# Kernel optimization log

Hardware: AMD Instinct MI355X
Metric: run time of the kernel (lower is better)

Reference implementation:

```python
import jax, jax.numpy as jnp
import numpy as np

B, N_ATOM, N_TOK = 1, 1536, 384
C_ATOM, C_PAIR, C_TOK = 128, 16, 384
C_HID, H, L = 32, 4, 3
HID = 2 * C_ATOM  # n_transition = 2
N_QUERY, N_KEY, INF = 32, 128, 1e9


def _ln(x, gamma=None, beta=None, eps=1e-5):
    mu = jnp.mean(x, axis=-1, keepdims=True)
    var = jnp.mean(jnp.square(x - mu), axis=-1, keepdims=True)
    y = (x - mu) * jax.lax.rsqrt(var + eps)
    if gamma is not None:
        y = y * gamma
    if beta is not None:
        y = y + beta
    return y


def _adaln(a, s, gamma_s, Wg, bg, Ws):
    an = _ln(a)            # LN without affine
    sn = _ln(s, gamma_s)   # scale-only LN
    return jax.nn.sigmoid(sn @ Wg + bg) * an + sn @ Ws


def _block_mask():
    # AtomTransformer.forward: 32-query x 128-key block-local mask
    offset = N_QUERY // 2 - 0.5
    n_center = N_ATOM // N_QUERY + 1
    centers = offset + jnp.arange(n_center, dtype=jnp.float32) * N_QUERY
    idx = jnp.arange(N_ATOM, dtype=jnp.float32)[:, None]
    row = (jnp.abs(idx - centers[None, :]) < N_QUERY / 2).astype(jnp.float32)
    col = (jnp.abs(idx - centers[None, :]) < N_KEY / 2).astype(jnp.float32)
    return (row @ col.T - 1.0) * INF   # [N,N]: 0 in-window, -INF outside


def _forward(ref_pos, ref_mask, ref_element, ref_charge, ref_atom_name_chars,
             ref_space_uid, token_mask, atom_to_token_index,
             W_feats, W_ref_offset, W_inv_sq, W_valid, W_l, W_m,
             W_mlp1, W_mlp2, W_mlp3, W_out_tok,
             attn_ada_gamma_s, attn_ada_Wg, attn_ada_bg, attn_ada_Ws,
             Wq, bq, Wk, Wv, lnz_g, lnz_b, Wb, Wgate, Wo, Wsg, bsg,
             tr_ada_gamma_s, tr_ada_Wg, tr_ada_bg, tr_ada_Ws,
             tr_W1, tr_W2, tr_Wog, tr_bog, tr_Wout):
    # --- RefAtomFeatureEmbedder (AF3 Alg 5 lines 1-6) ---
    feats = jnp.concatenate([
        ref_pos, ref_mask[..., None], ref_element, ref_charge[..., None],
        ref_atom_name_chars.reshape(B, N_ATOM, -1), ref_space_uid[..., None]], axis=-1)
    cl = feats @ W_feats                                     # [B,N,C_ATOM]
    d = ref_pos[:, None, :, :] - ref_pos[:, :, None, :]      # d[l,m] = pos[m]-pos[l]
    v = (ref_space_uid[:, None, :] == ref_space_uid[:, :, None]).astype(jnp.float32)[..., None]
    plm = (d @ W_ref_offset) * v
    inv_sq = 1.0 / (1.0 + jnp.sum(d * d, axis=-1, keepdims=True))
    plm = plm + (inv_sq @ W_inv_sq) * v + (v @ W_valid) * v  # [B,N,N,C_PAIR]
    ql = cl
    # --- single -> pair conditioning + pair MLP ---
    crelu = jax.nn.relu(cl)
    plm = plm + (crelu @ W_l)[:, :, None, :] + (crelu @ W_m)[:, None, :, :]
    h = jax.nn.relu(plm) @ W_mlp1
    h = jax.nn.relu(h) @ W_mlp2
    h = jax.nn.relu(h) @ W_mlp3
    plm = plm + h
    # --- AtomTransformer (Alg 7) -> DiffusionTransformer (Alg 23) ---
    beta = _block_mask()                                     # [N,N]
    atom_mask = jnp.einsum('blt,bt->bl', atom_to_token_index, token_mask)
    mask_bias = (atom_mask - 1.0)[:, None, None, :] * INF    # [B,1,1,N]
    a, s = ql, cl
    inv_sqrt = 1.0 / np.sqrt(C_HID)
    for i in range(L):
        # AttentionPairBias (Alg 24)
        an = _adaln(a, s, attn_ada_gamma_s[i], attn_ada_Wg[i], attn_ada_bg[i], attn_ada_Ws[i])
        q = (an @ Wq[i] + bq[i]).reshape(B, N_ATOM, H, C_HID)
        k = (an @ Wk[i]).reshape(B, N_ATOM, H, C_HID)
        vv = (an @ Wv[i]).reshape(B, N_ATOM, H, C_HID)
        zb = _ln(plm, lnz_g[i], lnz_b[i]) @ Wb[i]            # [B,N,N,H]
        logits = (jnp.einsum('bqhc,bkhc->bhqk', q, k) * inv_sqrt
                  + jnp.moveaxis(zb, -1, 1) + beta[None, None] + mask_bias)
        A = jax.nn.softmax(logits, axis=-1)
        o = jnp.einsum('bhqk,bkhc->bqhc', A, vv)
        g = jax.nn.sigmoid(an @ Wgate[i]).reshape(B, N_ATOM, H, C_HID)
        o = (g * o).reshape(B, N_ATOM, H * C_HID) @ Wo[i]
        attn_out = jax.nn.sigmoid(s @ Wsg[i] + bsg[i]) * o
        # ConditionedTransitionBlock (Alg 25) on pre-attention a (Alg 23)
        tn = _adaln(a, s, tr_ada_gamma_s[i], tr_ada_Wg[i], tr_ada_bg[i], tr_ada_Ws[i])
        hh = jax.nn.silu(tn @ tr_W1[i]) * (tn @ tr_W2[i])
        tr_out = jax.nn.sigmoid(s @ tr_Wog[i] + tr_bog[i]) * (hh @ tr_Wout[i])
        a = attn_out + tr_out
    # --- mean-aggregate atoms -> tokens (Alg 5 line 15) ---
    al = jax.nn.relu(a @ W_out_tok)                          # [B,N,C_TOK]
    counts = jnp.maximum(jnp.sum(atom_to_token_index, axis=1), 1.0)
    a_tok = jnp.einsum('blt,blc->btc', atom_to_token_index, al) / counts[..., None]
    return a_tok


def setup_inputs() -> dict:
    key = jax.random.key(0)
    ks = iter(jax.random.split(key, 80))

    def nrm(shape, scale=0.02):
        return jax.random.normal(next(ks), shape, dtype=jnp.float32) * scale

    inp = {}
    inp['ref_pos'] = jax.random.normal(next(ks), (B, N_ATOM, 3), dtype=jnp.float32) * 3.0
    inp['ref_mask'] = jnp.ones((B, N_ATOM), jnp.float32)
    elem = jax.random.randint(next(ks), (B, N_ATOM), 0, 128)
    inp['ref_element'] = jax.nn.one_hot(elem, 128, dtype=jnp.float32)
    inp['ref_charge'] = jax.random.normal(next(ks), (B, N_ATOM), dtype=jnp.float32)
    chars = jax.random.randint(next(ks), (B, N_ATOM, 4), 0, 64)
    inp['ref_atom_name_chars'] = jax.nn.one_hot(chars, 64, dtype=jnp.float32)
    inp['ref_space_uid'] = jnp.broadcast_to(
        (jnp.arange(N_ATOM) // 8).astype(jnp.float32), (B, N_ATOM))
    inp['token_mask'] = jnp.ones((B, N_TOK), jnp.float32)
    tok = (jnp.arange(N_ATOM) * N_TOK) // N_ATOM  # ~4 atoms per token
    inp['atom_to_token_index'] = jnp.broadcast_to(
        jax.nn.one_hot(tok, N_TOK, dtype=jnp.float32), (B, N_ATOM, N_TOK))
    # embedder params
    inp['W_feats'] = nrm((390, C_ATOM))
    inp['W_ref_offset'] = nrm((3, C_PAIR))
    inp['W_inv_sq'] = nrm((1, C_PAIR))
    inp['W_valid'] = nrm((1, C_PAIR))
    inp['W_l'] = nrm((C_ATOM, C_PAIR))
    inp['W_m'] = nrm((C_ATOM, C_PAIR))
    inp['W_mlp1'] = nrm((C_PAIR, C_PAIR))
    inp['W_mlp2'] = nrm((C_PAIR, C_PAIR))
    inp['W_mlp3'] = nrm((C_PAIR, C_PAIR))
    inp['W_out_tok'] = nrm((C_ATOM, C_TOK))
    # DiffusionTransformer params, stacked over L blocks
    inp['attn_ada_gamma_s'] = jnp.ones((L, C_ATOM), jnp.float32)
    inp['attn_ada_Wg'] = nrm((L, C_ATOM, C_ATOM))
    inp['attn_ada_bg'] = jnp.zeros((L, C_ATOM), jnp.float32)
    inp['attn_ada_Ws'] = nrm((L, C_ATOM, C_ATOM))
    inp['Wq'] = nrm((L, C_ATOM, H * C_HID))
    inp['bq'] = jnp.zeros((L, H * C_HID), jnp.float32)
    inp['Wk'] = nrm((L, C_ATOM, H * C_HID))
    inp['Wv'] = nrm((L, C_ATOM, H * C_HID))
    inp['lnz_g'] = jnp.ones((L, C_PAIR), jnp.float32)
    inp['lnz_b'] = jnp.zeros((L, C_PAIR), jnp.float32)
    inp['Wb'] = nrm((L, C_PAIR, H))
    inp['Wgate'] = nrm((L, C_ATOM, H * C_HID))
    inp['Wo'] = nrm((L, H * C_HID, C_ATOM))
    inp['Wsg'] = nrm((L, C_ATOM, C_ATOM))
    inp['bsg'] = jnp.full((L, C_ATOM), -2.0, jnp.float32)
    inp['tr_ada_gamma_s'] = jnp.ones((L, C_ATOM), jnp.float32)
    inp['tr_ada_Wg'] = nrm((L, C_ATOM, C_ATOM))
    inp['tr_ada_bg'] = jnp.zeros((L, C_ATOM), jnp.float32)
    inp['tr_ada_Ws'] = nrm((L, C_ATOM, C_ATOM))
    inp['tr_W1'] = nrm((L, C_ATOM, HID))
    inp['tr_W2'] = nrm((L, C_ATOM, HID))
    inp['tr_Wog'] = nrm((L, C_ATOM, C_ATOM))
    inp['tr_bog'] = jnp.full((L, C_ATOM), -2.0, jnp.float32)
    inp['tr_Wout'] = nrm((L, HID, C_ATOM))
    return inp


def reference(ref_pos, ref_mask, ref_element, ref_charge, ref_atom_name_chars,
              ref_space_uid, token_mask, atom_to_token_index,
              W_feats, W_ref_offset, W_inv_sq, W_valid, W_l, W_m,
              W_mlp1, W_mlp2, W_mlp3, W_out_tok,
              attn_ada_gamma_s, attn_ada_Wg, attn_ada_bg, attn_ada_Ws,
              Wq, bq, Wk, Wv, lnz_g, lnz_b, Wb, Wgate, Wo, Wsg, bsg,
              tr_ada_gamma_s, tr_ada_Wg, tr_ada_bg, tr_ada_Ws,
              tr_W1, tr_W2, tr_Wog, tr_bog, tr_Wout):
    return _forward(ref_pos, ref_mask, ref_element, ref_charge, ref_atom_name_chars,
                    ref_space_uid, token_mask, atom_to_token_index,
                    W_feats, W_ref_offset, W_inv_sq, W_valid, W_l, W_m,
                    W_mlp1, W_mlp2, W_mlp3, W_out_tok,
                    attn_ada_gamma_s, attn_ada_Wg, attn_ada_bg, attn_ada_Ws,
                    Wq, bq, Wk, Wv, lnz_g, lnz_b, Wb, Wgate, Wo, Wsg, bsg,
                    tr_ada_gamma_s, tr_ada_Wg, tr_ada_bg, tr_ada_Ws,
                    tr_W1, tr_W2, tr_Wog, tr_bog, tr_Wout)
```

## Files before the change

kernel.cpp:

```cpp
#include <hip/hip_runtime.h>
#include <math.h>

#define N_ATOM 1536
#define NB     48
#define NLAYER 3
#define NC     196608L
#define ZSTRIDE 786432L

struct GD { const float* A; const float* B; float* C; const float* ks; const float* bias;
            int act; int ldb; int ldc; int _pad; };
struct GB { GD g[18]; };

__global__ __launch_bounds__(128) void embed_tok_kernel(
    const float* __restrict__ pos, const float* __restrict__ rmask,
    const float* __restrict__ elem, const float* __restrict__ charge,
    const float* __restrict__ chars, const float* __restrict__ uid,
    const float* __restrict__ Wf, const float* __restrict__ W_l, const float* __restrict__ W_m,
    const float* __restrict__ a2t, const float* __restrict__ tmask,
    float* __restrict__ cl, float* __restrict__ aa, float* __restrict__ clnorm,
    float* __restrict__ pl, float* __restrict__ pm,
    int* __restrict__ tok, float* __restrict__ amask)
{
  int l = blockIdx.x, c = threadIdx.x;
  __shared__ int sidx[6];
  __shared__ float red[128];
  __shared__ float crow[128];
  if (elem[(long)l * 128 + c] > 0.5f) sidx[0] = c;
  float v0 = chars[(long)l * 256 + c];
  if (v0 > 0.5f) sidx[1 + (c >> 6)] = c & 63;
  float v1 = chars[(long)l * 256 + 128 + c];
  if (v1 > 0.5f) sidx[3 + (c >> 6)] = c & 63;
  for (int j = c; j < 384; j += 128)
    if (a2t[(long)l * 384 + j] > 0.5f) sidx[5] = j;
  __syncthreads();
  float acc = pos[l * 3 + 0] * Wf[c]
            + pos[l * 3 + 1] * Wf[128 + c]
            + pos[l * 3 + 2] * Wf[256 + c]
            + rmask[l] * Wf[384 + c]
            + Wf[(4 + sidx[0]) * 128 + c]
            + charge[l] * Wf[132 * 128 + c]
            + Wf[(133 + sidx[1]) * 128 + c]
            + Wf[(197 + sidx[2]) * 128 + c]
            + Wf[(261 + sidx[3]) * 128 + c]
            + Wf[(325 + sidx[4]) * 128 + c]
            + uid[l] * Wf[389 * 128 + c];
  long gi = (long)l * 128 + c;
  cl[gi] = acc; aa[gi] = acc; crow[c] = fmaxf(acc, 0.f);
  red[c] = acc; __syncthreads();
  for (int s = 64; s > 0; s >>= 1) { if (c < s) red[c] += red[c + s]; __syncthreads(); }
  float mu = red[0] * (1.f / 128.f); __syncthreads();
  float d = acc - mu; red[c] = d * d; __syncthreads();
  for (int s = 64; s > 0; s >>= 1) { if (c < s) red[c] += red[c + s]; __syncthreads(); }
  clnorm[gi] = d * rsqrtf(red[0] * (1.f / 128.f) + 1e-5f);
  if (c < 32) {
    const float* W = (c < 16) ? W_l : W_m;
    int o = c & 15;
    float s = 0.f;
    for (int cc = 0; cc < 128; cc++) s = fmaf(crow[cc], W[cc * 16 + o], s);
    if (c < 16) pl[l * 16 + o] = s; else pm[l * 16 + o] = s;
  }
  if (c == 127) {
    int j = sidx[5];
    tok[l] = j; amask[l] = tmask[j];
  }
}

__global__ __launch_bounds__(128) void adaln_kernel(
    const float* __restrict__ a,
    const float* __restrict__ sgA, const float* __restrict__ adA,
    const float* __restrict__ sgT, const float* __restrict__ adT,
    float* __restrict__ an, float* __restrict__ tn)
{
  __shared__ float red[128];
  int l = blockIdx.x, c = threadIdx.x;
  float x = a[(long)l * 128 + c];
  red[c] = x; __syncthreads();
  for (int s = 64; s > 0; s >>= 1) { if (c < s) red[c] += red[c + s]; __syncthreads(); }
  float mu = red[0] * (1.f / 128.f); __syncthreads();
  float d = x - mu; red[c] = d * d; __syncthreads();
  for (int s = 64; s > 0; s >>= 1) { if (c < s) red[c] += red[c + s]; __syncthreads(); }
  float nv = d * rsqrtf(red[0] * (1.f / 128.f) + 1e-5f);
  long i = (long)l * 128 + c;
  an[i] = sgA[i] * nv + adA[i];
  tn[i] = sgT[i] * nv + adT[i];
}

__device__ __forceinline__ void gemm64_body(float* sm, const float* A, const float* B, float* C,
                                            const float* ks, const float* bias, int act,
                                            int ldb, int ldc, int row0, int col0) {
  float* As = sm; float* Bs = sm + 2176;
  int tid = threadIdx.x;
  int tx = tid & 15, ty = tid >> 4;
  float acc[4][4] = {};
  for (int k0 = 0; k0 < 128; k0 += 32) {
    __syncthreads();
    { int r = tid >> 3, k4 = tid & 7;
#pragma unroll
      for (int half = 0; half < 2; half++) {
        int row = r + half * 32;
        float4 v = *(const float4*)(A + (long)(row0 + row) * 128 + k0 + k4 * 4);
        if (ks) { const float* kp = ks + k0 + k4 * 4; v.x *= kp[0]; v.y *= kp[1]; v.z *= kp[2]; v.w *= kp[3]; }
        As[(k4 * 4 + 0) * 68 + row] = v.x; As[(k4 * 4 + 1) * 68 + row] = v.y;
        As[(k4 * 4 + 2) * 68 + row] = v.z; As[(k4 * 4 + 3) * 68 + row] = v.w;
      } }
    { int kk = tid >> 4, n4 = tid & 15;
#pragma unroll
      for (int half = 0; half < 2; half++) {
        int k = kk + half * 16;
        *(float4*)&Bs[k * 68 + n4 * 4] = *(const float4*)(B + (long)(k0 + k) * ldb + col0 + n4 * 4);
      } }
    __syncthreads();
#pragma unroll
    for (int kk = 0; kk < 32; kk++) {
      float4 a = *(const float4*)&As[kk * 68 + ty * 4];
      float4 b = *(const float4*)&Bs[kk * 68 + tx * 4];
      float av[4] = {a.x, a.y, a.z, a.w}, bv[4] = {b.x, b.y, b.z, b.w};
#pragma unroll
      for (int i = 0; i < 4; i++)
#pragma unroll
        for (int j = 0; j < 4; j++) acc[i][j] = fmaf(av[i], bv[j], acc[i][j]);
    }
  }
  __syncthreads();
#pragma unroll
  for (int i = 0; i < 4; i++) {
    int row = row0 + ty * 4 + i;
#pragma unroll
    for (int j = 0; j < 4; j++) {
      int col = col0 + tx * 4 + j;
      float x = acc[i][j];
      if (bias) x += bias[col];
      if (act == 1) x = 1.f / (1.f + expf(-x));
      else if (act == 2) x = fmaxf(x, 0.f);
      C[(long)row * ldc + col] = x;
    }
  }
}

__global__ __launch_bounds__(256) void gemm64(GB args, int M)
{
  __shared__ float sm[4352];
  GD d = args.g[blockIdx.z];
  gemm64_body(sm, d.A, d.B, d.C, d.ks, d.bias, d.act, d.ldb, d.ldc, blockIdx.y * 64, blockIdx.x * 64);
}

__global__ __launch_bounds__(256) void zpre_kernel(
    const float* __restrict__ pos, const float* __restrict__ uid,
    const float* __restrict__ Wro, const float* __restrict__ Winv, const float* __restrict__ Wval,
    const float* __restrict__ M1, const float* __restrict__ M2, const float* __restrict__ M3,
    const float* __restrict__ Lg, const float* __restrict__ Lb, const float* __restrict__ Wb,
    const float* __restrict__ pl, const float* __restrict__ pm, float* __restrict__ zb,
    GB ba)
{
  __shared__ float sm[4352];
  int bid = blockIdx.x, tid = threadIdx.x;
  if (bid >= 768) {
    int u = bid - 768;
    GD d = ba.g[u / 48];
    int tt = u % 48;
    gemm64_body(sm, d.A, d.B, d.C, d.ks, d.bias, d.act, d.ldb, d.ldc, (tt >> 1) * 64, (tt & 1) * 64);
    return;
  }
  if (tid < 48)  sm[tid] = Wro[tid];
  if (tid < 16)  { sm[48 + tid] = Winv[tid]; sm[64 + tid] = Wval[tid]; }
  sm[80 + tid] = M1[tid]; sm[336 + tid] = M2[tid]; sm[592 + tid] = M3[tid];
  if (tid < 48)  { sm[848 + tid] = Lg[tid]; sm[896 + tid] = Lb[tid]; }
  if (tid < 192) sm[944 + tid] = Wb[tid];
  __syncthreads();
  const float* sWro = sm;      const float* sWinv = sm + 48;  const float* sWval = sm + 64;
  const float* sM1 = sm + 80;  const float* sM2 = sm + 336;   const float* sM3 = sm + 592;
  const float* sLg = sm + 848; const float* sLb = sm + 896;   const float* sWb = sm + 944;
  int b = bid >> 4;
  int pc = (bid & 15) * 256 + tid;
  int qi = pc >> 7, kj = pc & 127;
  int l = b * 32 + qi, m = b * 32 - 48 + kj;
  long base = (long)(b * 32 + qi) * 128 + kj;
  if (m < 0 || m >= N_ATOM) {
    for (int i = 0; i < NLAYER; i++)
      for (int h = 0; h < 4; h++) zb[i * ZSTRIDE + h * NC + base] = 0.f;
    return;
  }
  float dx = pos[m * 3 + 0] - pos[l * 3 + 0];
  float dy = pos[m * 3 + 1] - pos[l * 3 + 1];
  float dz = pos[m * 3 + 2] - pos[l * 3 + 2];
  float v = (uid[m] == uid[l]) ? 1.f : 0.f;
  float inv = 1.f / (1.f + dx * dx + dy * dy + dz * dz);
  float pv[16], ha[16], hb[16];
#pragma unroll
  for (int j = 0; j < 16; j++)
    pv[j] = v * (dx * sWro[j] + dy * sWro[16 + j] + dz * sWro[32 + j] + inv * sWinv[j] + sWval[j])
            + pl[l * 16 + j] + pm[m * 16 + j];
#pragma unroll
  for (int jo = 0; jo < 16; jo++) { float s = 0.f; for (int ji = 0; ji < 16; ji++) s = fmaf(fmaxf(pv[ji], 0.f), sM1[ji * 16 + jo], s); ha[jo] = s; }
#pragma unroll
  for (int jo = 0; jo < 16; jo++) { float s = 0.f; for (int ji = 0; ji < 16; ji++) s = fmaf(fmaxf(ha[ji], 0.f), sM2[ji * 16 + jo], s); hb[jo] = s; }
#pragma unroll
  for (int jo = 0; jo < 16; jo++) { float s = 0.f; for (int ji = 0; ji < 16; ji++) s = fmaf(fmaxf(hb[ji], 0.f), sM3[ji * 16 + jo], s); ha[jo] = s; }
#pragma unroll
  for (int j = 0; j < 16; j++) pv[j] += ha[j];
  for (int i = 0; i < NLAYER; i++) {
    float mu = 0.f;
#pragma unroll
    for (int j = 0; j < 16; j++) mu += pv[j];
    mu *= (1.f / 16.f);
    float var = 0.f;
#pragma unroll
    for (int j = 0; j < 16; j++) { float dd = pv[j] - mu; var += dd * dd; }
    var *= (1.f / 16.f);
    float rs = rsqrtf(var + 1e-5f);
    float zn[16];
#pragma unroll
    for (int j = 0; j < 16; j++) zn[j] = (pv[j] - mu) * rs * sLg[i * 16 + j] + sLb[i * 16 + j];
    for (int h = 0; h < 4; h++) {
      float s = 0.f;
#pragma unroll
      for (int j = 0; j < 16; j++) s = fmaf(zn[j], sWb[i * 64 + j * 4 + h], s);
      zb[i * ZSTRIDE + h * NC + base] = s;
    }
  }
}

__global__ __launch_bounds__(256) void attn_kernel(
    const float* __restrict__ qb, const float* __restrict__ kb, const float* __restrict__ vb,
    const float* __restrict__ gb, const float* __restrict__ zb, const float* __restrict__ amask,
    float* __restrict__ go)
{
  __shared__ float qs[16][36], ks[128][36], vs[128][36], ps[16][132];
  int bx = blockIdx.x, h = blockIdx.y, t = threadIdx.x;
  int b = bx >> 1, half = bx & 1;
  int q0 = b * 32 + half * 16;
  int kbase = b * 32 - 48;
  const float* zbh = zb + (long)h * NC;
  if (t < 128) {
    int qi = t >> 3, c4 = t & 7;
    *(float4*)&qs[qi][c4 * 4] = *(const float4*)(qb + (long)(q0 + qi) * 128 + h * 32 + c4 * 4);
  }
  for (int idx = t; idx < 128 * 8; idx += 256) {
    int kj = idx >> 3, c4 = idx & 7;
    int m = kbase + kj;
    float4 kv = make_float4(0.f, 0.f, 0.f, 0.f), vv = make_float4(0.f, 0.f, 0.f, 0.f);
    if (m >= 0 && m < N_ATOM) {
      kv = *(const float4*)(kb + (long)m * 128 + h * 32 + c4 * 4);
      vv = *(const float4*)(vb + (long)m * 128 + h * 32 + c4 * 4);
    }
    *(float4*)&ks[kj][c4 * 4] = kv;
    *(float4*)&vs[kj][c4 * 4] = vv;
  }
  __syncthreads();
  const float isq = 0.17677669529663687f;
  for (int p = t; p < 2048; p += 256) {
    int qi = p >> 7, kj = p & 127;
    int m = kbase + kj;
    float s = 0.f;
#pragma unroll
    for (int c4 = 0; c4 < 8; c4++) {
      float4 a = *(const float4*)&qs[qi][c4 * 4];
      float4 k4 = *(const float4*)&ks[kj][c4 * 4];
      s = fmaf(a.x, k4.x, s); s = fmaf(a.y, k4.y, s);
      s = fmaf(a.z, k4.z, s); s = fmaf(a.w, k4.w, s);
    }
    float logit;
    if (m >= 0 && m < N_ATOM) {
      logit = s * isq + zbh[(long)(q0 + qi) * 128 + kj] + (amask[m] - 1.f) * 1e9f;
    } else {
      logit = -1e9f;
    }
    ps[qi][kj] = logit;
  }
  __syncthreads();
  {
    int row = t >> 4, ln = t & 15;
    float mx = -1e30f;
    for (int kj = ln; kj < 128; kj += 16) mx = fmaxf(mx, ps[row][kj]);
#pragma unroll
    for (int o = 8; o > 0; o >>= 1) mx = fmaxf(mx, __shfl_xor(mx, o));
    float sm = 0.f;
    for (int kj = ln; kj < 128; kj += 16) { float e = expf(ps[row][kj] - mx); ps[row][kj] = e; sm += e; }
#pragma unroll
    for (int o = 8; o > 0; o >>= 1) sm += __shfl_xor(sm, o);
    float r = 1.f / sm;
    for (int kj = ln; kj < 128; kj += 16) ps[row][kj] *= r;
  }
  __syncthreads();
  {
    int qi = t >> 4, seg = (t >> 3) & 1, c4 = t & 7;
    float4 acc = make_float4(0.f, 0.f, 0.f, 0.f);
    int kj0 = seg * 64;
#pragma unroll 4
    for (int kj = kj0; kj < kj0 + 64; kj++) {
      float p = ps[qi][kj];
      float4 v = *(const float4*)&vs[kj][c4 * 4];
      acc.x = fmaf(p, v.x, acc.x); acc.y = fmaf(p, v.y, acc.y);
      acc.z = fmaf(p, v.z, acc.z); acc.w = fmaf(p, v.w, acc.w);
    }
    acc.x += __shfl_xor(acc.x, 8);
    acc.y += __shfl_xor(acc.y, 8);
    acc.z += __shfl_xor(acc.z, 8);
    acc.w += __shfl_xor(acc.w, 8);
    if (seg == 0) {
      long gi = (long)(q0 + qi) * 128 + h * 32 + c4 * 4;
      float4 g = *(const float4*)(gb + gi);
      acc.x *= g.x; acc.y *= g.y; acc.z *= g.z; acc.w *= g.w;
      *(float4*)(go + gi) = acc;
    }
  }
}

__global__ __launch_bounds__(256) void gemm_dual32(
    const float* __restrict__ A1, const float* __restrict__ B1,
    const float* __restrict__ h1, const float* __restrict__ h2, const float* __restrict__ B2,
    const float* __restrict__ g1, const float* __restrict__ g2,
    float* __restrict__ C)
{
  __shared__ float As[32 * 36];
  __shared__ float Bs[32 * 68];
  const int N = 128;
  int t = threadIdx.x;
  int row0 = blockIdx.y * 32, col0 = blockIdx.x * 64;
  int tx = t & 15, ty = t >> 4;
  float acc1[2][4] = {}, acc2[2][4] = {};
  for (int k0 = 0; k0 < 128; k0 += 32) {
    __syncthreads();
    { int r = t >> 3, k4 = t & 7;
      float4 v = *(const float4*)(A1 + (long)(row0 + r) * 128 + k0 + k4 * 4);
      As[(k4 * 4 + 0) * 36 + r] = v.x; As[(k4 * 4 + 1) * 36 + r] = v.y;
      As[(k4 * 4 + 2) * 36 + r] = v.z; As[(k4 * 4 + 3) * 36 + r] = v.w;
    }
    for (int e = t; e < 512; e += 256) {
      int k = e >> 4, n4 = e & 15;
      *(float4*)&Bs[k * 68 + n4 * 4] = *(const float4*)(B1 + (long)(k0 + k) * N + col0 + n4 * 4);
    }
    __syncthreads();
#pragma unroll
    for (int kk = 0; kk < 32; kk++) {
      float a0 = As[kk * 36 + ty * 2], a1 = As[kk * 36 + ty * 2 + 1];
      float4 b = *(const float4*)&Bs[kk * 68 + tx * 4];
      float bv[4] = {b.x, b.y, b.z, b.w};
#pragma unroll
      for (int j = 0; j < 4; j++) {
        acc1[0][j] = fmaf(a0, bv[j], acc1[0][j]);
        acc1[1][j] = fmaf(a1, bv[j], acc1[1][j]);
      }
    }
  }
  for (int k0 = 0; k0 < 256; k0 += 32) {
    __syncthreads();
    { int r = t >> 3, k4 = t & 7;
      long o = (long)(row0 + r) * 256 + k0 + k4 * 4;
      float4 x = *(const float4*)(h1 + o);
      float4 y = *(const float4*)(h2 + o);
      As[(k4 * 4 + 0) * 36 + r] = (x.x / (1.f + expf(-x.x))) * y.x;
      As[(k4 * 4 + 1) * 36 + r] = (x.y / (1.f + expf(-x.y))) * y.y;
      As[(k4 * 4 + 2) * 36 + r] = (x.z / (1.f + expf(-x.z))) * y.z;
      As[(k4 * 4 + 3) * 36 + r] = (x.w / (1.f + expf(-x.w))) * y.w;
    }
    for (int e = t; e < 512; e += 256) {
      int k = e >> 4, n4 = e & 15;
      *(float4*)&Bs[k * 68 + n4 * 4] = *(const float4*)(B2 + (long)(k0 + k) * N + col0 + n4 * 4);
    }
    __syncthreads();
#pragma unroll
    for (int kk = 0; kk < 32; kk++) {
      float a0 = As[kk * 36 + ty * 2], a1 = As[kk * 36 + ty * 2 + 1];
      float4 b = *(const float4*)&Bs[kk * 68 + tx * 4];
      float bv[4] = {b.x, b.y, b.z, b.w};
#pragma unroll
      for (int j = 0; j < 4; j++) {
        acc2[0][j] = fmaf(a0, bv[j], acc2[0][j]);
        acc2[1][j] = fmaf(a1, bv[j], acc2[1][j]);
      }
    }
  }
#pragma unroll
  for (int i = 0; i < 2; i++) {
    long o = (long)(row0 + ty * 2 + i) * N + col0 + tx * 4;
    float4 ga = *(const float4*)(g1 + o);
    float4 gb = *(const float4*)(g2 + o);
    float4 r;
    r.x = ga.x * acc1[i][0] + gb.x * acc2[i][0];
    r.y = ga.y * acc1[i][1] + gb.y * acc2[i][1];
    r.z = ga.z * acc1[i][2] + gb.z * acc2[i][2];
    r.w = ga.w * acc1[i][3] + gb.w * acc2[i][3];
    *(float4*)(C + o) = r;
  }
}

__global__ __launch_bounds__(256) void gemm_scatter(
    const float* __restrict__ A, const float* __restrict__ B,
    const int* __restrict__ tok,
    float* __restrict__ out, int K)
{
  __shared__ float As[32][68];
  __shared__ float Bs[32][68];
  int tid = threadIdx.x;
  int row0 = blockIdx.y * 64, col0 = blockIdx.x * 64;
  int tx = tid & 15, ty = tid >> 4;
  float acc[4][4] = {};
  for (int k0 = 0; k0 < K; k0 += 32) {
    __syncthreads();
    { int r = tid >> 3, k4 = tid & 7;
#pragma unroll
      for (int half = 0; half < 2; half++) {
        int row = r + half * 32;
        float4 v = *(const float4*)(A + (long)(row0 + row) * K + k0 + k4 * 4);
        As[k4 * 4 + 0][row] = v.x; As[k4 * 4 + 1][row] = v.y;
        As[k4 * 4 + 2][row] = v.z; As[k4 * 4 + 3][row] = v.w;
      } }
    { int kk = tid >> 4, n4 = tid & 15;
#pragma unroll
      for (int half = 0; half < 2; half++) {
        int k = kk + half * 16;
        float4 v = *(const float4*)(B + (long)(k0 + k) * 384 + col0 + n4 * 4);
        *(float4*)&Bs[k][n4 * 4] = v;
      } }
    __syncthreads();
#pragma unroll
    for (int kk = 0; kk < 32; kk++) {
      float4 a = *(const float4*)&As[kk][ty * 4];
      float4 b = *(const float4*)&Bs[kk][tx * 4];
      float av[4] = {a.x, a.y, a.z, a.w}, bv[4] = {b.x, b.y, b.z, b.w};
#pragma unroll
      for (int i = 0; i < 4; i++)
#pragma unroll
        for (int j = 0; j < 4; j++) acc[i][j] = fmaf(av[i], bv[j], acc[i][j]);
    }
  }
  __syncthreads();
  int r0 = row0 + ty * 4;
  int t0 = tok[r0];
  int cnt = 0;
#pragma unroll
  for (int i = 0; i < 4; i++) cnt += (tok[r0 + i] == t0) ? 1 : 0;
  float inv = 1.f / fmaxf((float)cnt, 1.f);
#pragma unroll
  for (int j = 0; j < 4; j++) {
    int col = col0 + tx * 4 + j;
    float s = 0.f;
#pragma unroll
    for (int i = 0; i < 4; i++)
      if (tok[r0 + i] == t0) s += fmaxf(acc[i][j], 0.f);
    out[(long)t0 * 384 + col] = s * inv;
  }
}

extern "C" void kernel_launch(void* const* d_in, const int* in_sizes, int n_in,
                              void* d_out, int out_size, void* d_ws, size_t ws_size,
                              hipStream_t stream)
{
  const float* pos    = (const float*)d_in[0];
  const float* rmask  = (const float*)d_in[1];
  const float* elem   = (const float*)d_in[2];
  const float* charge = (const float*)d_in[3];
  const float* chars  = (const float*)d_in[4];
  const float* uid    = (const float*)d_in[5];
  const float* tmask  = (const float*)d_in[6];
  const float* a2t    = (const float*)d_in[7];
  const float* Wf     = (const float*)d_in[8];
  const float* Wro    = (const float*)d_in[9];
  const float* Winv   = (const float*)d_in[10];
  const float* Wval   = (const float*)d_in[11];
  const float* W_l    = (const float*)d_in[12];
  const float* W_m    = (const float*)d_in[13];
  const float* M1     = (const float*)d_in[14];
  const float* M2     = (const float*)d_in[15];
  const float* M3     = (const float*)d_in[16];
  const float* Wtok   = (const float*)d_in[17];
  const float* gA     = (const float*)d_in[18];
  const float* WgA    = (const float*)d_in[19];
  const float* bgA    = (const float*)d_in[20];
  const float* WsA    = (const float*)d_in[21];
  const float* Wq     = (const float*)d_in[22];
  const float* bq     = (const float*)d_in[23];
  const float* Wk     = (const float*)d_in[24];
  const float* Wv     = (const float*)d_in[25];
  const float* Lg     = (const float*)d_in[26];
  const float* Lb     = (const float*)d_in[27];
  const float* Wb     = (const float*)d_in[28];
  const float* Wgate  = (const float*)d_in[29];
  const float* Wo     = (const float*)d_in[30];
  const float* Wsg    = (const float*)d_in[31];
  const float* bsg    = (const float*)d_in[32];
  const float* gT     = (const float*)d_in[33];
  const float* WgT    = (const float*)d_in[34];
  const float* bgT    = (const float*)d_in[35];
  const float* WsT    = (const float*)d_in[36];
  const float* trW1   = (const float*)d_in[37];
  const float* trW2   = (const float*)d_in[38];
  const float* Wog    = (const float*)d_in[39];
  const float* bog    = (const float*)d_in[40];
  const float* Wout   = (const float*)d_in[41];
  float* out = (float*)d_out;

  float* ws = (float*)d_ws;
  size_t off = 0;
  auto alloc = [&](size_t n) { float* p = ws + off; off += n; return p; };
  float* cl     = alloc(NC);
  float* aa     = alloc(NC);
  float* clnorm = alloc(NC);
  float* an     = alloc(NC);
  float* tn     = alloc(NC);
  float* qbuf   = alloc(NC);
  float* kbuf   = alloc(NC);
  float* vbuf   = alloc(NC);
  float* gbuf   = alloc(NC);
  float* gobuf  = alloc(NC);
  float* h1     = alloc((size_t)N_ATOM * 256);
  float* h2     = alloc((size_t)N_ATOM * 256);
  float* pl     = alloc((size_t)N_ATOM * 16);
  float* pm     = alloc((size_t)N_ATOM * 16);
  float* zbias  = alloc((size_t)NLAYER * ZSTRIDE);
  float* sgA    = alloc(NC * NLAYER);
  float* adA    = alloc(NC * NLAYER);
  float* sgT    = alloc(NC * NLAYER);
  float* adT    = alloc(NC * NLAYER);
  float* gsg    = alloc(NC * NLAYER);
  float* gog    = alloc(NC * NLAYER);
  float* amask  = alloc(N_ATOM);
  int*   tok    = (int*)alloc(N_ATOM);
  (void)ws_size; (void)in_sizes; (void)n_in; (void)out_size;

  embed_tok_kernel<<<N_ATOM, 128, 0, stream>>>(pos, rmask, elem, charge, chars, uid, Wf,
                                               W_l, W_m, a2t, tmask,
                                               cl, aa, clnorm, pl, pm, tok, amask);

  {
    GB ba = {};
    for (int i = 0; i < NLAYER; i++) {
      size_t o = (size_t)i * NC;
      ba.g[i * 6 + 0] = { clnorm, WgA + i * 16384, sgA + o, gA + i * 128, bgA + i * 128, 1, 128, 128, 0 };
      ba.g[i * 6 + 1] = { clnorm, WsA + i * 16384, adA + o, gA + i * 128, nullptr,       0, 128, 128, 0 };
      ba.g[i * 6 + 2] = { clnorm, WgT + i * 16384, sgT + o, gT + i * 128, bgT + i * 128, 1, 128, 128, 0 };
      ba.g[i * 6 + 3] = { clnorm, WsT + i * 16384, adT + o, gT + i * 128, nullptr,       0, 128, 128, 0 };
      ba.g[i * 6 + 4] = { cl,     Wsg + i * 16384, gsg + o, nullptr,      bsg + i * 128, 1, 128, 128, 0 };
      ba.g[i * 6 + 5] = { cl,     Wog + i * 16384, gog + o, nullptr,      bog + i * 128, 1, 128, 128, 0 };
    }
    zpre_kernel<<<768 + 864, 256, 0, stream>>>(pos, uid, Wro, Winv, Wval, M1, M2, M3,
                                               Lg, Lb, Wb, pl, pm, zbias, ba);
  }

  for (int i = 0; i < NLAYER; i++) {
    size_t o = (size_t)i * NC;
    adaln_kernel<<<N_ATOM, 128, 0, stream>>>(aa, sgA + o, adA + o, sgT + o, adT + o, an, tn);
    {
      GB ba = {};
      ba.g[0] = { an, Wq + i * 16384,        qbuf, nullptr, bq + i * 128, 0, 128, 128, 0 };
      ba.g[1] = { an, Wk + i * 16384,        kbuf, nullptr, nullptr,      0, 128, 128, 0 };
      ba.g[2] = { an, Wv + i * 16384,        vbuf, nullptr, nullptr,      0, 128, 128, 0 };
      ba.g[3] = { an, Wgate + i * 16384,     gbuf, nullptr, nullptr,      1, 128, 128, 0 };
      ba.g[4] = { tn, trW1 + i * 32768,       h1,  nullptr, nullptr,      0, 256, 256, 0 };
      ba.g[5] = { tn, trW1 + i * 32768 + 128, h1 + 128, nullptr, nullptr, 0, 256, 256, 0 };
      ba.g[6] = { tn, trW2 + i * 32768,       h2,  nullptr, nullptr,      0, 256, 256, 0 };
      ba.g[7] = { tn, trW2 + i * 32768 + 128, h2 + 128, nullptr, nullptr, 0, 256, 256, 0 };
      gemm64<<<dim3(2, 24, 8), 256, 0, stream>>>(ba, N_ATOM);
    }
    attn_kernel<<<dim3(96, 4), 256, 0, stream>>>(qbuf, kbuf, vbuf, gbuf,
                                                 zbias + (size_t)i * ZSTRIDE, amask, gobuf);
    gemm_dual32<<<dim3(2, 48), 256, 0, stream>>>(gobuf, Wo + i * 16384, h1, h2, Wout + i * 32768,
                                                 gsg + o, gog + o, aa);
  }

  gemm_scatter<<<dim3(6, 24), 256, 0, stream>>>(aa, Wtok, tok, out, 128);
}
```

Measured before the change: 338.5 us.

## Fuse LayerNorm and AdaLN modulation into GEMM A-tile load

Removes the standalone adaln kernel and the clnorm precompute. The GEMM now loads the full 64x128 A tile once, computes per-row LayerNorm with warp shuffles, optionally applies the sg/ad modulation, and stores it into an XOR-swizzled shared layout. The K loop also moves from 32-wide to 64-wide steps. This saves three kernel launches and the an/tn round trips through global memory, but the LN statistics are now recomputed by every column tile and by all 8 GEMMs per layer. Shared memory per block grows to about 51KB, which may reduce occupancy, including in zpre_kernel.

```diff
diff --git a/kernel.cpp b/kernel.cpp
--- a/kernel.cpp
+++ b/kernel.cpp
@@ -2,13 +2,12 @@
 #include <math.h>
 
 #define N_ATOM 1536
-#define NB     48
 #define NLAYER 3
 #define NC     196608L
 #define ZSTRIDE 786432L
 
 struct GD { const float* A; const float* B; float* C; const float* ks; const float* bias;
-            int act; int ldb; int ldc; int _pad; };
+            const float* sg; const float* ad; int act; int ldb; int ldc; int mode; };
 struct GB { GD g[18]; };
 
 __global__ __launch_bounds__(128) void embed_tok_kernel(
@@ -17,13 +16,12 @@
     const float* __restrict__ chars, const float* __restrict__ uid,
     const float* __restrict__ Wf, const float* __restrict__ W_l, const float* __restrict__ W_m,
     const float* __restrict__ a2t, const float* __restrict__ tmask,
-    float* __restrict__ cl, float* __restrict__ aa, float* __restrict__ clnorm,
+    float* __restrict__ cl, float* __restrict__ aa,
     float* __restrict__ pl, float* __restrict__ pm,
     int* __restrict__ tok, float* __restrict__ amask)
 {
   int l = blockIdx.x, c = threadIdx.x;
   __shared__ int sidx[6];
-  __shared__ float red[128];
   __shared__ float crow[128];
   if (elem[(long)l * 128 + c] > 0.5f) sidx[0] = c;
   float v0 = chars[(long)l * 256 + c];
@@ -46,12 +44,7 @@
             + uid[l] * Wf[389 * 128 + c];
   long gi = (long)l * 128 + c;
   cl[gi] = acc; aa[gi] = acc; crow[c] = fmaxf(acc, 0.f);
-  red[c] = acc; __syncthreads();
-  for (int s = 64; s > 0; s >>= 1) { if (c < s) red[c] += red[c + s]; __syncthreads(); }
-  float mu = red[0] * (1.f / 128.f); __syncthreads();
-  float d = acc - mu; red[c] = d * d; __syncthreads();
-  for (int s = 64; s > 0; s >>= 1) { if (c < s) red[c] += red[c + s]; __syncthreads(); }
-  clnorm[gi] = d * rsqrtf(red[0] * (1.f / 128.f) + 1e-5f);
+  __syncthreads();
   if (c < 32) {
     const float* W = (c < 16) ? W_l : W_m;
     int o = c & 15;
@@ -65,54 +58,69 @@
   }
 }
 
-__global__ __launch_bounds__(128) void adaln_kernel(
-    const float* __restrict__ a,
-    const float* __restrict__ sgA, const float* __restrict__ adA,
-    const float* __restrict__ sgT, const float* __restrict__ adT,
-    float* __restrict__ an, float* __restrict__ tn)
-{
-  __shared__ float red[128];
-  int l = blockIdx.x, c = threadIdx.x;
-  float x = a[(long)l * 128 + c];
-  red[c] = x; __syncthreads();
-  for (int s = 64; s > 0; s >>= 1) { if (c < s) red[c] += red[c + s]; __syncthreads(); }
-  float mu = red[0] * (1.f / 128.f); __syncthreads();
-  float d = x - mu; red[c] = d * d; __syncthreads();
-  for (int s = 64; s > 0; s >>= 1) { if (c < s) red[c] += red[c + s]; __syncthreads(); }
-  float nv = d * rsqrtf(red[0] * (1.f / 128.f) + 1e-5f);
-  long i = (long)l * 128 + c;
-  an[i] = sgA[i] * nv + adA[i];
-  tn[i] = sgT[i] * nv + adT[i];
-}
-
-__device__ __forceinline__ void gemm64_body(float* sm, const float* A, const float* B, float* C,
-                                            const float* ks, const float* bias, int act,
-                                            int ldb, int ldc, int row0, int col0) {
-  float* As = sm; float* Bs = sm + 2176;
-  int tid = threadIdx.x;
-  int tx = tid & 15, ty = tid >> 4;
+__device__ __forceinline__ void gemm64_body(float* sm, const GD d, int row0, int col0) {
+  float* As = sm;
+  float* Bs = sm + 8704;
+  int t = threadIdx.x;
+  {
+    int sub = t >> 5, lane = t & 31;
+#pragma unroll
+    for (int it = 0; it < 8; it++) {
+      int row = it * 8 + sub;
+      long gro = (long)(row0 + row) * 128 + lane * 4;
+      float4 v = *(const float4*)(d.A + gro);
+      float vals[4] = {v.x, v.y, v.z, v.w};
+      if (d.mode >= 1) {
+        float s1 = vals[0] + vals[1] + vals[2] + vals[3];
+#pragma unroll
+        for (int o = 16; o; o >>= 1) s1 += __shfl_xor(s1, o);
+        float mu = s1 * (1.f / 128.f);
+        float s2 = 0.f;
+#pragma unroll
+        for (int cc = 0; cc < 4; cc++) { float dd = vals[cc] - mu; s2 += dd * dd; }
+#pragma unroll
+        for (int o = 16; o; o >>= 1) s2 += __shfl_xor(s2, o);
+        float rs = rsqrtf(s2 * (1.f / 128.f) + 1e-5f);
+        if (d.mode == 2) {
+          float4 sg4 = *(const float4*)(d.sg + gro);
+          float4 ad4 = *(const float4*)(d.ad + gro);
+          float sgv[4] = {sg4.x, sg4.y, sg4.z, sg4.w};
+          float adv[4] = {ad4.x, ad4.y, ad4.z, ad4.w};
+#pragma unroll
+          for (int cc = 0; cc < 4; cc++)
+            vals[cc] = fmaf(sgv[cc], (vals[cc] - mu) * rs, adv[cc]);
+        } else {
+#pragma unroll
+          for (int cc = 0; cc < 4; cc++) vals[cc] = (vals[cc] - mu) * rs;
+        }
+      }
+      if (d.ks) {
+        const float* kp = d.ks + lane * 4;
+#pragma unroll
+        for (int cc = 0; cc < 4; cc++) vals[cc] *= kp[cc];
+      }
+      int rg = row >> 2, rl = row & 3;
+#pragma unroll
+      for (int cc = 0; cc < 4; cc++) {
+        int k = lane * 4 + cc;
+        As[k * 68 + ((rg ^ (k & 15)) << 2) + rl] = vals[cc];
+      }
+    }
+  }
+  int tx = t & 15, ty = t >> 4;
   float acc[4][4] = {};
-  for (int k0 = 0; k0 < 128; k0 += 32) {
-    __syncthreads();
-    { int r = tid >> 3, k4 = tid & 7;
-#pragma unroll
-      for (int half = 0; half < 2; half++) {
-        int row = r + half * 32;
-        float4 v = *(const float4*)(A + (long)(row0 + row) * 128 + k0 + k4 * 4);
-        if (ks) { const float* kp = ks + k0 + k4 * 4; v.x *= kp[0]; v.y *= kp[1]; v.z *= kp[2]; v.w *= kp[3]; }
-        As[(k4 * 4 + 0) * 68 + row] = v.x; As[(k4 * 4 + 1) * 68 + row] = v.y;
-        As[(k4 * 4 + 2) * 68 + row] = v.z; As[(k4 * 4 + 3) * 68 + row] = v.w;
-      } }
-    { int kk = tid >> 4, n4 = tid & 15;
-#pragma unroll
-      for (int half = 0; half < 2; half++) {
-        int k = kk + half * 16;
-        *(float4*)&Bs[k * 68 + n4 * 4] = *(const float4*)(B + (long)(k0 + k) * ldb + col0 + n4 * 4);
-      } }
-    __syncthreads();
-#pragma unroll
-    for (int kk = 0; kk < 32; kk++) {
-      float4 a = *(const float4*)&As[kk * 68 + ty * 4];
+  for (int k0 = 0; k0 < 128; k0 += 64) {
+    __syncthreads();
+#pragma unroll
+    for (int it = 0; it < 4; it++) {
+      int k = it * 16 + (t >> 4), n4 = t & 15;
+      *(float4*)&Bs[k * 68 + n4 * 4] = *(const float4*)(d.B + (long)(k0 + k) * d.ldb + col0 + n4 * 4);
+    }
+    __syncthreads();
+#pragma unroll 16
+    for (int kk = 0; kk < 64; kk++) {
+      int ka = k0 + kk;
+      float4 a = *(const float4*)&As[ka * 68 + ((ty ^ (ka & 15)) << 2)];
       float4 b = *(const float4*)&Bs[kk * 68 + tx * 4];
       float av[4] = {a.x, a.y, a.z, a.w}, bv[4] = {b.x, b.y, b.z, b.w};
 #pragma unroll
@@ -121,7 +129,6 @@
         for (int j = 0; j < 4; j++) acc[i][j] = fmaf(av[i], bv[j], acc[i][j]);
     }
   }
-  __syncthreads();
 #pragma unroll
   for (int i = 0; i < 4; i++) {
     int row = row0 + ty * 4 + i;
@@ -129,19 +136,18 @@
     for (int j = 0; j < 4; j++) {
       int col = col0 + tx * 4 + j;
       float x = acc[i][j];
-      if (bias) x += bias[col];
-      if (act == 1) x = 1.f / (1.f + expf(-x));
-      else if (act == 2) x = fmaxf(x, 0.f);
-      C[(long)row * ldc + col] = x;
-    }
-  }
-}
-
-__global__ __launch_bounds__(256) void gemm64(GB args, int M)
-{
-  __shared__ float sm[4352];
-  GD d = args.g[blockIdx.z];
-  gemm64_body(sm, d.A, d.B, d.C, d.ks, d.bias, d.act, d.ldb, d.ldc, blockIdx.y * 64, blockIdx.x * 64);
+      if (d.bias) x += d.bias[col];
+      if (d.act == 1) x = 1.f / (1.f + expf(-x));
+      else if (d.act == 2) x = fmaxf(x, 0.f);
+      d.C[(long)row * d.ldc + col] = x;
+    }
+  }
+}
+
+__global__ __launch_bounds__(256) void gemm64(GB args)
+{
+  __shared__ float sm[13056];
+  gemm64_body(sm, args.g[blockIdx.z], blockIdx.y * 64, blockIdx.x * 64);
 }
 
 __global__ __launch_bounds__(256) void zpre_kernel(
@@ -152,13 +158,13 @@
     const float* __restrict__ pl, const float* __restrict__ pm, float* __restrict__ zb,
     GB ba)
 {
-  __shared__ float sm[4352];
+  __shared__ float sm[13056];
   int bid = blockIdx.x, tid = threadIdx.x;
   if (bid >= 768) {
     int u = bid - 768;
     GD d = ba.g[u / 48];
     int tt = u % 48;
-    gemm64_body(sm, d.A, d.B, d.C, d.ks, d.bias, d.act, d.ldb, d.ldc, (tt >> 1) * 64, (tt & 1) * 64);
+    gemm64_body(sm, d, (tt >> 1) * 64, (tt & 1) * 64);
     return;
   }
   if (tid < 48)  sm[tid] = Wro[tid];
@@ -496,9 +502,6 @@
   auto alloc = [&](size_t n) { float* p = ws + off; off += n; return p; };
   float* cl     = alloc(NC);
   float* aa     = alloc(NC);
-  float* clnorm = alloc(NC);
-  float* an     = alloc(NC);
-  float* tn     = alloc(NC);
   float* qbuf   = alloc(NC);
   float* kbuf   = alloc(NC);
   float* vbuf   = alloc(NC);
@@ -521,18 +524,18 @@
 
   embed_tok_kernel<<<N_ATOM, 128, 0, stream>>>(pos, rmask, elem, charge, chars, uid, Wf,
                                                W_l, W_m, a2t, tmask,
-                                               cl, aa, clnorm, pl, pm, tok, amask);
+                                               cl, aa, pl, pm, tok, amask);
 
   {
     GB ba = {};
     for (int i = 0; i < NLAYER; i++) {
       size_t o = (size_t)i * NC;
-      ba.g[i * 6 + 0] = { clnorm, WgA + i * 16384, sgA + o, gA + i * 128, bgA + i * 128, 1, 128, 128, 0 };
-      ba.g[i * 6 + 1] = { clnorm, WsA + i * 16384, adA + o, gA + i * 128, nullptr,       0, 128, 128, 0 };
-      ba.g[i * 6 + 2] = { clnorm, WgT + i * 16384, sgT + o, gT + i * 128, bgT + i * 128, 1, 128, 128, 0 };
-      ba.g[i * 6 + 3] = { clnorm, WsT + i * 16384, adT + o, gT + i * 128, nullptr,       0, 128, 128, 0 };
-      ba.g[i * 6 + 4] = { cl,     Wsg + i * 16384, gsg + o, nullptr,      bsg + i * 128, 1, 128, 128, 0 };
-      ba.g[i * 6 + 5] = { cl,     Wog + i * 16384, gog + o, nullptr,      bog + i * 128, 1, 128, 128, 0 };
+      ba.g[i * 6 + 0] = { cl, WgA + i * 16384, sgA + o, gA + i * 128, bgA + i * 128, nullptr, nullptr, 1, 128, 128, 1 };
+      ba.g[i * 6 + 1] = { cl, WsA + i * 16384, adA + o, gA + i * 128, nullptr,       nullptr, nullptr, 0, 128, 128, 1 };
+      ba.g[i * 6 + 2] = { cl, WgT + i * 16384, sgT + o, gT + i * 128, bgT + i * 128, nullptr, nullptr, 1, 128, 128, 1 };
+      ba.g[i * 6 + 3] = { cl, WsT + i * 16384, adT + o, gT + i * 128, nullptr,       nullptr, nullptr, 0, 128, 128, 1 };
+      ba.g[i * 6 + 4] = { cl, Wsg + i * 16384, gsg + o, nullptr,      bsg + i * 128, nullptr, nullptr, 1, 128, 128, 0 };
+      ba.g[i * 6 + 5] = { cl, Wog + i * 16384, gog + o, nullptr,      bog + i * 128, nullptr, nullptr, 1, 128, 128, 0 };
     }
     zpre_kernel<<<768 + 864, 256, 0, stream>>>(pos, uid, Wro, Winv, Wval, M1, M2, M3,
                                                Lg, Lb, Wb, pl, pm, zbias, ba);
@@ -540,18 +543,17 @@
 
   for (int i = 0; i < NLAYER; i++) {
     size_t o = (size_t)i * NC;
-    adaln_kernel<<<N_ATOM, 128, 0, stream>>>(aa, sgA + o, adA + o, sgT + o, adT + o, an, tn);
     {
       GB ba = {};
-      ba.g[0] = { an, Wq + i * 16384,        qbuf, nullptr, bq + i * 128, 0, 128, 128, 0 };
-      ba.g[1] = { an, Wk + i * 16384,        kbuf, nullptr, nullptr,      0, 128, 128, 0 };
-      ba.g[2] = { an, Wv + i * 16384,        vbuf, nullptr, nullptr,      0, 128, 128, 0 };
-      ba.g[3] = { an, Wgate + i * 16384,     gbuf, nullptr, nullptr,      1, 128, 128, 0 };
-      ba.g[4] = { tn, trW1 + i * 32768,       h1,  nullptr, nullptr,      0, 256, 256, 0 };
-      ba.g[5] = { tn, trW1 + i * 32768 + 128, h1 + 128, nullptr, nullptr, 0, 256, 256, 0 };
-      ba.g[6] = { tn, trW2 + i * 32768,       h2,  nullptr, nullptr,      0, 256, 256, 0 };
-      ba.g[7] = { tn, trW2 + i * 32768 + 128, h2 + 128, nullptr, nullptr, 0, 256, 256, 0 };
-      gemm64<<<dim3(2, 24, 8), 256, 0, stream>>>(ba, N_ATOM);
+      ba.g[0] = { aa, Wq + i * 16384,        qbuf,     nullptr, bq + i * 128, sgA + o, adA + o, 0, 128, 128, 2 };
+      ba.g[1] = { aa, Wk + i * 16384,        kbuf,     nullptr, nullptr,      sgA + o, adA + o, 0, 128, 128, 2 };
+      ba.g[2] = { aa, Wv + i * 16384,        vbuf,     nullptr, nullptr,      sgA + o, adA + o, 0, 128, 128, 2 };
+      ba.g[3] = { aa, Wgate + i * 16384,     gbuf,     nullptr, nullptr,      sgA + o, adA + o, 1, 128, 128, 2 };
+      ba.g[4] = { aa, trW1 + i * 32768,       h1,      nullptr, nullptr,      sgT + o, adT + o, 0, 256, 256, 2 };
+      ba.g[5] = { aa, trW1 + i * 32768 + 128, h1 + 128, nullptr, nullptr,     sgT + o, adT + o, 0, 256, 256, 2 };
+      ba.g[6] = { aa, trW2 + i * 32768,       h2,      nullptr, nullptr,      sgT + o, adT + o, 0, 256, 256, 2 };
+      ba.g[7] = { aa, trW2 + i * 32768 + 128, h2 + 128, nullptr, nullptr,     sgT + o, adT + o, 0, 256, 256, 2 };
+      gemm64<<<dim3(2, 24, 8), 256, 0, stream>>>(ba);
     }
     attn_kernel<<<dim3(96, 4), 256, 0, stream>>>(qbuf, kbuf, vbuf, gbuf,
                                                  zbias + (size_t)i * ZSTRIDE, amask, gobuf);
```

Result: slower. 378.5 us (+11.8%).
